# Kernel optimization log

Hardware: AMD Instinct MI355X
Metric: run time of the kernel (lower is better)

## Reference

```python
import jax, jax.numpy as jnp
import numpy as np

N = 50000       # nodes
E = 800000      # directed edges (src -> dst)
INDIM, HID, OUT = 256, 128, 64
NEG_SLOPE = 0.2  # PyG GATConv default negative_slope


def gat_layer(x, src, dst, W, a_src, a_dst, b, n_nodes):
    """Single-head PyG-style GATConv with self-loops already in (src, dst)."""
    h = x @ W.T                                   # [N, F_out]
    alpha_src = h @ a_src                         # [N]
    alpha_dst = h @ a_dst                         # [N]
    # per-edge attention logits, LeakyReLU
    e = jax.nn.leaky_relu(alpha_src[src] + alpha_dst[dst], NEG_SLOPE)  # [E']
    # segment softmax grouped by destination node (numerically stable)
    m = jnp.full((n_nodes,), -jnp.inf, e.dtype).at[dst].max(e)
    ee = jnp.exp(e - m[dst])
    denom = jax.ops.segment_sum(ee, dst, num_segments=n_nodes)
    alpha = ee / denom[dst]                       # [E']
    # weighted scatter-add of source messages
    out = jax.ops.segment_sum(h[src] * alpha[:, None], dst, num_segments=n_nodes)
    return out + b


def setup_inputs() -> dict:
    key = jax.random.key(0)
    ks = jax.random.split(key, 10)
    s = 0.1
    return {
        "x": jax.random.normal(ks[0], (N, INDIM), jnp.float32),
        "edge_index": jax.random.randint(ks[1], (2, E), 0, N, dtype=jnp.int32),
        "W1": jax.random.normal(ks[2], (HID, INDIM), jnp.float32) * s,
        "a_src1": jax.random.normal(ks[3], (HID,), jnp.float32) * s,
        "a_dst1": jax.random.normal(ks[4], (HID,), jnp.float32) * s,
        "b1": jnp.zeros((HID,), jnp.float32),
        "W2": jax.random.normal(ks[5], (OUT, HID), jnp.float32) * s,
        "a_src2": jax.random.normal(ks[6], (OUT,), jnp.float32) * s,
        "a_dst2": jax.random.normal(ks[7], (OUT,), jnp.float32) * s,
        "b2": jnp.zeros((OUT,), jnp.float32),
    }


def reference(x, edge_index, W1, a_src1, a_dst1, b1, W2, a_src2, a_dst2, b2):
    n_nodes = x.shape[0]
    # PyG GATConv default add_self_loops=True
    loops = jnp.arange(n_nodes, dtype=edge_index.dtype)
    src = jnp.concatenate([edge_index[0], loops])
    dst = jnp.concatenate([edge_index[1], loops])
    h = gat_layer(x, src, dst, W1, a_src1, a_dst1, b1, n_nodes)
    h = jax.nn.relu(h)
    h = gat_layer(h, src, dst, W2, a_src2, a_dst2, b2, n_nodes)
    return h
```

## Files before the change

kernel.cpp:

```cpp
#include <hip/hip_runtime.h>
#include <hip/hip_bf16.h>
#include <math.h>

#define NN 50000
#define EE 800000
#define INDIM 256
#define HID 128
#define OUTF 64
#define NEG_SLOPE 0.2f
#define CAP 64

#define NB ((NN + 255) >> 8)
#define BCAP 6144
#define CHUNK 2048
#define EPT 8
#define BPAD 16

typedef __attribute__((ext_vector_type(8))) short bf16x8;
typedef __attribute__((ext_vector_type(4))) float f32x4;

__device__ inline float bflo(unsigned p) { return __uint_as_float(p << 16); }
__device__ inline float bfhi(unsigned p) { return __uint_as_float(p & 0xffff0000u); }
__device__ inline unsigned f2bf(float f) {
    unsigned u = __float_as_uint(f);
    return (u + 0x7fffu + ((u >> 16) & 1u)) >> 16;
}
__device__ inline unsigned cvt_pk_bf16(float lo, float hi) {
    unsigned r;
    asm("v_cvt_pk_bf16_f32 %0, %1, %2" : "=v"(r) : "v"(lo), "v"(hi));
    return r;
}
__device__ inline float leaky(float l) { return (l > 0.f) ? l : NEG_SLOPE * l; }

template <typename AT, int BM, int BN, int WR, int WC, bool FAL>
__device__ inline void gemm_body(const AT* __restrict__ A,
                                 const float* __restrict__ B,
                                 unsigned short* __restrict__ Cb,
                                 const float* __restrict__ a_s,
                                 const float* __restrict__ a_d,
                                 float* __restrict__ asrc,
                                 float* __restrict__ adst,
                                 int N, int K, int bid)
{
    constexpr int LD = 40;
    constexpr int MF = (BM / WR) / 16;
    constexpr int NF = (BN / WC) / 16;
    constexpr int NA  = (sizeof(AT) == 4) ? (BM * 8 / 256) : (BM * 4 / 256);
    constexpr int NBL = BN * 8 / 256;
    __shared__ unsigned short As[BM * LD];
    __shared__ unsigned short Bs[BN * LD];
    __shared__ float al_s[FAL ? 2 * BM : 2];

    const int tid = threadIdx.x;
    const int wave = tid >> 6, lane = tid & 63;
    const int wr = wave / WC, wc = wave % WC;
    const int wrow0 = wr * (BM / WR);
    const int wcol0 = wc * (BN / WC);
    const int row0 = bid * BM;
    const int lrow = lane & 15, lkg = lane >> 4;

    if constexpr (FAL) {
        for (int i = tid; i < 2 * BM; i += 256) al_s[i] = 0.f;
    }

    int arow[NA], aoff[NA]; bool aval[NA];
    #pragma unroll
    for (int u = 0; u < NA; ++u) {
        int i = u * 256 + tid;
        if constexpr (sizeof(AT) == 4) { arow[u] = i >> 3; aoff[u] = (i & 7) * 4; }
        else                           { arow[u] = i >> 2; aoff[u] = (i & 3) * 8; }
        aval[u] = (row0 + arow[u]) < N;
    }
    int brow[NBL], boff[NBL];
    #pragma unroll
    for (int u = 0; u < NBL; ++u) {
        int i = u * 256 + tid;
        brow[u] = i >> 3; boff[u] = (i & 7) * 4;
    }

    uint4 ra[NA], rb[NBL];
    auto loadA = [&](int k0) {
        #pragma unroll
        for (int u = 0; u < NA; ++u) {
            ra[u] = make_uint4(0u, 0u, 0u, 0u);
            if (aval[u])
                ra[u] = *(const uint4*)((const AT*)A + (size_t)(row0 + arow[u]) * K + k0 + aoff[u]);
        }
    };
    auto loadB = [&](int k0) {
        #pragma unroll
        for (int u = 0; u < NBL; ++u)
            rb[u] = *(const uint4*)(B + (size_t)brow[u] * K + k0 + boff[u]);
    };
    auto storeLDS = [&]() {
        if constexpr (sizeof(AT) == 4) {
            #pragma unroll
            for (int u = 0; u < NA; ++u) {
                unsigned p0 = cvt_pk_bf16(__uint_as_float(ra[u].x), __uint_as_float(ra[u].y));
                unsigned p1 = cvt_pk_bf16(__uint_as_float(ra[u].z), __uint_as_float(ra[u].w));
                *(uint2*)&As[arow[u] * LD + aoff[u]] = make_uint2(p0, p1);
            }
        } else {
            #pragma unroll
            for (int u = 0; u < NA; ++u)
                *(uint4*)&As[arow[u] * LD + aoff[u]] = ra[u];
        }
        #pragma unroll
        for (int u = 0; u < NBL; ++u) {
            unsigned p0 = cvt_pk_bf16(__uint_as_float(rb[u].x), __uint_as_float(rb[u].y));
            unsigned p1 = cvt_pk_bf16(__uint_as_float(rb[u].z), __uint_as_float(rb[u].w));
            *(uint2*)&Bs[brow[u] * LD + boff[u]] = make_uint2(p0, p1);
        }
    };

    f32x4 acc[MF][NF];
    #pragma unroll
    for (int mi = 0; mi < MF; ++mi)
        #pragma unroll
        for (int ni = 0; ni < NF; ++ni) acc[mi][ni] = 0.f;

    const int NK = K / 32;
    loadA(0); loadB(0);
    for (int ks = 0; ks < NK; ++ks) {
        storeLDS();
        __syncthreads();
        if (ks + 1 < NK) { loadA((ks + 1) * 32); loadB((ks + 1) * 32); }

        bf16x8 af[MF], bfr[NF];
        #pragma unroll
        for (int mi = 0; mi < MF; ++mi)
            af[mi] = *(const bf16x8*)&As[(wrow0 + mi * 16 + lrow) * LD + lkg * 8];
        #pragma unroll
        for (int ni = 0; ni < NF; ++ni)
            bfr[ni] = *(const bf16x8*)&Bs[(wcol0 + ni * 16 + lrow) * LD + lkg * 8];
        #pragma unroll
        for (int mi = 0; mi < MF; ++mi)
            #pragma unroll
            for (int ni = 0; ni < NF; ++ni)
                acc[mi][ni] = __builtin_amdgcn_mfma_f32_16x16x32_bf16(
                    af[mi], bfr[ni], acc[mi][ni], 0, 0, 0);
        __syncthreads();
    }

    if constexpr (FAL) {
        float asv[NF], adv[NF];
        #pragma unroll
        for (int ni = 0; ni < NF; ++ni) {
            int c = wcol0 + ni * 16 + lrow;
            asv[ni] = a_s[c]; adv[ni] = a_d[c];
        }
        #pragma unroll
        for (int mi = 0; mi < MF; ++mi)
            #pragma unroll
            for (int r = 0; r < 4; ++r) {
                float ps = 0.f, pd = 0.f;
                #pragma unroll
                for (int ni = 0; ni < NF; ++ni) {
                    ps = fmaf(acc[mi][ni][r], asv[ni], ps);
                    pd = fmaf(acc[mi][ni][r], adv[ni], pd);
                }
                #pragma unroll
                for (int d = 1; d < 16; d <<= 1) {
                    ps += __shfl_xor(ps, d);
                    pd += __shfl_xor(pd, d);
                }
                int lr_ = wrow0 + mi * 16 + lkg * 4 + r;
                if (lrow == 0) {
                    atomicAdd(&al_s[lr_], ps);
                    atomicAdd(&al_s[BM + lr_], pd);
                }
            }
    }

    #pragma unroll
    for (int mi = 0; mi < MF; ++mi)
        #pragma unroll
        for (int ni = 0; ni < NF; ++ni)
            #pragma unroll
            for (int r = 0; r < 4; ++r) {
                int gr = row0 + wrow0 + mi * 16 + lkg * 4 + r;
                int gc = wcol0 + ni * 16 + lrow;
                if (gr < N)
                    Cb[(size_t)gr * BN + gc] = (unsigned short)f2bf(acc[mi][ni][r]);
            }

    if constexpr (FAL) {
        __syncthreads();
        if (tid < BM) {
            int gr = row0 + tid;
            if (gr < N) { asrc[gr] = al_s[tid]; adst[gr] = al_s[BM + tid]; }
        }
    }
}

__device__ inline void bin_body(int bb,
                                const int* __restrict__ src_in,
                                const int* __restrict__ dst_in,
                                unsigned* __restrict__ gbucket,
                                int* __restrict__ bcnt,
                                int E, int tot)
{
    __shared__ int h_hist[256];
    __shared__ int h_scan[256];
    __shared__ int h_ofs[256];
    __shared__ int h_gbase[256];
    __shared__ unsigned grp[CHUNK];

    const int tid = threadIdx.x;
    const int e0 = bb * CHUNK;
    const int cntc = min(CHUNK, tot - e0);

    h_hist[tid] = 0;
    __syncthreads();

    unsigned pk[EPT];
    bool val[EPT];
    #pragma unroll
    for (int u = 0; u < EPT; ++u) {
        int e = e0 + u * 256 + tid;
        val[u] = (e < tot);
        if (val[u]) {
            int d, s;
            if (e < E) { d = dst_in[e]; s = src_in[e]; }
            else       { d = e - E;    s = d; }
            pk[u] = ((unsigned)d << 16) | (unsigned)s;
            atomicAdd(&h_hist[d >> 8], 1);
        }
    }
    __syncthreads();

    int v = h_hist[tid];
    int incl = v;
    h_scan[tid] = incl;
    __syncthreads();
    for (int off = 1; off < 256; off <<= 1) {
        int t = (tid >= off) ? h_scan[tid - off] : 0;
        __syncthreads();
        incl += t;
        h_scan[tid] = incl;
        __syncthreads();
    }
    int excl = incl - v;
    h_scan[tid] = excl;
    h_ofs[tid] = excl;
    h_gbase[tid] = (tid < NB && v > 0) ? atomicAdd(&bcnt[tid * BPAD], v) : 0;
    __syncthreads();

    #pragma unroll
    for (int u = 0; u < EPT; ++u)
        if (val[u]) {
            int b = pk[u] >> 24;
            int pos = atomicAdd(&h_ofs[b], 1);
            grp[pos] = pk[u];
        }
    __syncthreads();

    for (int i = tid; i < cntc; i += 256) {
        unsigned p = grp[i];
        int b = p >> 24;
        int gp = h_gbase[b] + (i - h_scan[b]);
        if (gp < BCAP) gbucket[(size_t)b * BCAP + gp] = p;
    }
}

__global__ __launch_bounds__(256) void fused_gemm1_bin(
    const float* __restrict__ x, const float* __restrict__ W1,
    unsigned short* __restrict__ h1b,
    const float* __restrict__ a_s, const float* __restrict__ a_d,
    float* __restrict__ asrc, float* __restrict__ adst,
    const int* __restrict__ src_in, const int* __restrict__ dst_in,
    unsigned* __restrict__ gbucket, int* __restrict__ bcnt,
    int N, int K, int GB, int E)
{
    if ((int)blockIdx.x < GB) {
        gemm_body<float, 64, 128, 2, 2, true>(x, W1, h1b, a_s, a_d,
                                              asrc, adst, N, K, blockIdx.x);
    } else {
        bin_body(blockIdx.x - GB, src_in, dst_in, gbucket, bcnt, E, E + N);
    }
}

__global__ __launch_bounds__(256) void csr_build(
    const unsigned* __restrict__ gbucket, const int* __restrict__ bcnt,
    int* __restrict__ cnt, unsigned short* __restrict__ csr, int N)
{
    __shared__ int c2[256];
    __shared__ unsigned short cl[256 * CAP];

    const int b = blockIdx.x;
    const int tid = threadIdx.x;
    c2[tid] = 0;
    __syncthreads();

    int len = bcnt[b * BPAD];
    if (len > BCAP) len = BCAP;
    for (int i = tid; i < len; i += 256) {
        unsigned p = gbucket[(size_t)b * BCAP + i];
        int dl = (p >> 16) & 255;
        int s  = p & 0xffff;
        int r = atomicAdd(&c2[dl], 1);
        if (r < CAP) cl[(dl << 6) + r] = (unsigned short)s;
    }
    __syncthreads();

    int d = (b << 8) + tid;
    if (d < N) cnt[d] = c2[tid];

    int rows = N - (b << 8);
    rows = (rows > 256) ? 256 : rows;
    const uint4* sp = (const uint4*)cl;
    uint4* dp = (uint4*)(csr + (((size_t)b << 8) << 6));
    for (int i = tid; i < rows * 8; i += 256) dp[i] = sp[i];
}

__global__ __launch_bounds__(256) void agg1_gemm2_kernel(
    const unsigned short* __restrict__ h1b, const unsigned short* __restrict__ csr,
    const int* __restrict__ cnt_arr, const float* __restrict__ asrc1,
    const float* __restrict__ adst1, const float* __restrict__ b1,
    const float* __restrict__ W2, const float* __restrict__ a_s2,
    const float* __restrict__ a_d2, unsigned short* __restrict__ h2b,
    float* __restrict__ asrc2, float* __restrict__ adst2, int N)
{
    constexpr int F = HID, G = 16, EPI = 4, STEP = 16;
    constexpr int LDH = 136;
    __shared__ unsigned short hm[64 * LDH];
    __shared__ unsigned short Bs[64 * 40];

    const int tid = threadIdx.x;
    const int wv = tid >> 6, lane = tid & 63;
    const int base = (int)blockIdx.x * 64;
    const int grp = lane / G, fl = lane % G;

    float bs[8];
    *(float4*)&bs[0] = *(const float4*)(b1 + fl * 8);
    *(float4*)&bs[4] = *(const float4*)(b1 + fl * 8 + 4);

    for (int i = 0; i < 16; ++i) {
        const int row = i * 4 + wv;
        const int node = base + row;
        float acc[8];
        #pragma unroll
        for (int p = 0; p < 8; ++p) acc[p] = 0.f;

        if (node < N) {
            const size_t beg = (size_t)node << 6;
            int cntv = cnt_arr[node];
            cntv = (cntv > CAP) ? CAP : cntv;
            const float ad = adst1[node];

            int s = 0;
            float e = 0.f;
            if (lane < cntv) { s = (int)csr[beg + lane]; e = __expf(leaky(asrc1[s] + ad)); }
            float denom = e;
            #pragma unroll
            for (int d = 32; d > 0; d >>= 1) denom += __shfl_xor(denom, d);
            float w = e * __fdividef(1.f, denom);

            for (int jj0 = 0; jj0 < cntv; jj0 += STEP) {
                uint4 q[4];
                float wj[4];
                #pragma unroll
                for (int u = 0; u < 4; ++u) {
                    int sel = jj0 + u * EPI + grp;
                    int sj = __shfl(s, sel);
                    wj[u] = __shfl(w, sel);
                    q[u] = make_uint4(0u, 0u, 0u, 0u);
                    if (sel < cntv)
                        q[u] = *(const uint4*)(h1b + (size_t)sj * F + fl * 8);
                }
                #pragma unroll
                for (int u = 0; u < 4; ++u) {
                    acc[0] += wj[u] * bflo(q[u].x); acc[1] += wj[u] * bfhi(q[u].x);
                    acc[2] += wj[u] * bflo(q[u].y); acc[3] += wj[u] * bfhi(q[u].y);
                    acc[4] += wj[u] * bflo(q[u].z); acc[5] += wj[u] * bfhi(q[u].z);
                    acc[6] += wj[u] * bflo(q[u].w); acc[7] += wj[u] * bfhi(q[u].w);
                }
            }
            #pragma unroll
            for (int d = G; d < 64; d <<= 1)
                #pragma unroll
                for (int p = 0; p < 8; ++p) acc[p] += __shfl_xor(acc[p], d);

            #pragma unroll
            for (int p = 0; p < 8; ++p) acc[p] = fmaxf(acc[p] + bs[p], 0.f);
        }
        if (lane < G) {
            uint4 pk;
            pk.x = cvt_pk_bf16(acc[0], acc[1]);
            pk.y = cvt_pk_bf16(acc[2], acc[3]);
            pk.z = cvt_pk_bf16(acc[4], acc[5]);
            pk.w = cvt_pk_bf16(acc[6], acc[7]);
            *(uint4*)&hm[row * LDH + lane * 8] = pk;
        }
    }
    __syncthreads();

    const int lrow = lane & 15, lkg = lane >> 4;
    f32x4 acc2[4];
    #pragma unroll
    for (int ni = 0; ni < 4; ++ni) acc2[ni] = 0.f;

    for (int k0 = 0; k0 < HID; k0 += 32) {
        #pragma unroll
        for (int it = tid; it < 64 * 8; it += 256) {
            int rw = it >> 3, kq = it & 7;
            float4 v = *(const float4*)(W2 + (size_t)rw * HID + k0 + kq * 4);
            unsigned p0 = cvt_pk_bf16(v.x, v.y);
            unsigned p1 = cvt_pk_bf16(v.z, v.w);
            *(uint2*)&Bs[rw * 40 + kq * 4] = make_uint2(p0, p1);
        }
        __syncthreads();
        bf16x8 af = *(const bf16x8*)&hm[(wv * 16 + lrow) * LDH + k0 + lkg * 8];
        #pragma unroll
        for (int ni = 0; ni < 4; ++ni) {
            bf16x8 bfr = *(const bf16x8*)&Bs[(ni * 16 + lrow) * 40 + lkg * 8];
            acc2[ni] = __builtin_amdgcn_mfma_f32_16x16x32_bf16(af, bfr, acc2[ni], 0, 0, 0);
        }
        __syncthreads();
    }

    float asv[4], adv[4];
    #pragma unroll
    for (int ni = 0; ni < 4; ++ni) {
        int c = ni * 16 + lrow;
        asv[ni] = a_s2[c]; adv[ni] = a_d2[c];
    }
    #pragma unroll
    for (int r = 0; r < 4; ++r) {
        float ps = 0.f, pd = 0.f;
        #pragma unroll
        for (int ni = 0; ni < 4; ++ni) {
            ps = fmaf(acc2[ni][r], asv[ni], ps);
            pd = fmaf(acc2[ni][r], adv[ni], pd);
        }
        #pragma unroll
        for (int d = 1; d < 16; d <<= 1) {
            ps += __shfl_xor(ps, d);
            pd += __shfl_xor(pd, d);
        }
        int gr = base + wv * 16 + lkg * 4 + r;
        if (lrow == 0 && gr < N) { asrc2[gr] = ps; adst2[gr] = pd; }
    }

    #pragma unroll
    for (int ni = 0; ni < 4; ++ni)
        #pragma unroll
        for (int r = 0; r < 4; ++r) {
            int gr = base + wv * 16 + lkg * 4 + r;
            int gc = ni * 16 + lrow;
            if (gr < N)
                h2b[(size_t)gr * OUTF + gc] = (unsigned short)f2bf(acc2[ni][r]);
        }
}

template <int F, bool RELU, bool OUTBF>
__global__ __launch_bounds__(256) void aggregate_kernel(
    const unsigned short* __restrict__ hb, const unsigned short* __restrict__ csr,
    const int* __restrict__ cnt_arr, const float* __restrict__ asrc,
    const float* __restrict__ adst, const float* __restrict__ bias,
    void* __restrict__ outv, int n)
{
    constexpr int G = F / 8;
    constexpr int EPI = 64 / G;
    constexpr int STEP = EPI * 4;
    int wave = (int)((blockIdx.x * (size_t)blockDim.x + threadIdx.x) >> 6);
    int lane = threadIdx.x & 63;
    if (wave >= n) return;
    const size_t beg = (size_t)wave << 6;
    int cntv = cnt_arr[wave];
    cntv = (cntv > CAP) ? CAP : cntv;
    const float ad = adst[wave];
    const int grp = lane / G, fl = lane % G;

    float acc[8];
    #pragma unroll
    for (int p = 0; p < 8; ++p) acc[p] = 0.f;

    int s = 0;
    float e = 0.f;
    if (lane < cntv) { s = (int)csr[beg + lane]; e = __expf(leaky(asrc[s] + ad)); }
    float denom = e;
    #pragma unroll
    for (int d = 32; d > 0; d >>= 1) denom += __shfl_xor(denom, d);
    float w = e * __fdividef(1.f, denom);

    for (int jj0 = 0; jj0 < cntv; jj0 += STEP) {
        uint4 q[4];
        float wj[4];
        #pragma unroll
        for (int u = 0; u < 4; ++u) {
            int sel = jj0 + u * EPI + grp;
            int sj = __shfl(s, sel);
            wj[u] = __shfl(w, sel);
            q[u] = make_uint4(0u, 0u, 0u, 0u);
            if (sel < cntv)
                q[u] = *(const uint4*)(hb + (size_t)sj * F + fl * 8);
        }
        #pragma unroll
        for (int u = 0; u < 4; ++u) {
            acc[0] += wj[u] * bflo(q[u].x); acc[1] += wj[u] * bfhi(q[u].x);
            acc[2] += wj[u] * bflo(q[u].y); acc[3] += wj[u] * bfhi(q[u].y);
            acc[4] += wj[u] * bflo(q[u].z); acc[5] += wj[u] * bfhi(q[u].z);
            acc[6] += wj[u] * bflo(q[u].w); acc[7] += wj[u] * bfhi(q[u].w);
        }
    }

    #pragma unroll
    for (int d = G; d < 64; d <<= 1)
        #pragma unroll
        for (int p = 0; p < 8; ++p) acc[p] += __shfl_xor(acc[p], d);

    if (lane < G) {
        float v[8];
        #pragma unroll
        for (int p = 0; p < 8; ++p) {
            v[p] = acc[p] + bias[fl * 8 + p];
            if (RELU) v[p] = fmaxf(v[p], 0.f);
        }
        if constexpr (OUTBF) {
            unsigned short* o = (unsigned short*)outv + (size_t)wave * F + fl * 8;
            uint4 pk;
            pk.x = cvt_pk_bf16(v[0], v[1]);
            pk.y = cvt_pk_bf16(v[2], v[3]);
            pk.z = cvt_pk_bf16(v[4], v[5]);
            pk.w = cvt_pk_bf16(v[6], v[7]);
            *(uint4*)o = pk;
        } else {
            float* o = (float*)outv + (size_t)wave * F + fl * 8;
            *(float4*)o       = make_float4(v[0], v[1], v[2], v[3]);
            *(float4*)(o + 4) = make_float4(v[4], v[5], v[6], v[7]);
        }
    }
}

extern "C" void kernel_launch(void* const* d_in, const int* in_sizes, int n_in,
                              void* d_out, int out_size, void* d_ws, size_t ws_size,
                              hipStream_t stream)
{
    const float* x      = (const float*)d_in[0];
    const int*   ei     = (const int*)d_in[1];
    const float* W1     = (const float*)d_in[2];
    const float* a_src1 = (const float*)d_in[3];
    const float* a_dst1 = (const float*)d_in[4];
    const float* b1     = (const float*)d_in[5];
    const float* W2     = (const float*)d_in[6];
    const float* a_src2 = (const float*)d_in[7];
    const float* a_dst2 = (const float*)d_in[8];
    const float* b2     = (const float*)d_in[9];
    float* out = (float*)d_out;

    const int N = NN, E = EE;
    const int* src_in = ei;
    const int* dst_in = ei + E;

    char* p = (char*)d_ws;
    unsigned short* h1b   = (unsigned short*)p; p += (size_t)N * HID * 2;
    unsigned short* h2b   = (unsigned short*)p; p += (size_t)N * OUTF * 2;
    float* asrc  = (float*)p; p += (size_t)N * 4;
    float* adst  = (float*)p; p += (size_t)N * 4;
    float* asrc2 = (float*)p; p += (size_t)N * 4;
    float* adst2 = (float*)p; p += (size_t)N * 4;
    int* cnt    = (int*)p;   p += (size_t)N * 4;
    unsigned short* csr = (unsigned short*)p; p += (size_t)N * CAP * 2;
    int* bcnt = (int*)p; p += (size_t)NB * BPAD * 4;
    unsigned* gbucket = (unsigned*)h2b;

    hipMemsetAsync(bcnt, 0, (size_t)NB * BPAD * 4, stream);

    const int GB   = (N + 63) / 64;
    const int BINB = (E + N + CHUNK - 1) / CHUNK;
    const int nwb  = (N * 64 + 255) / 256;

    fused_gemm1_bin<<<GB + BINB, 256, 0, stream>>>(
        x, W1, h1b, a_src1, a_dst1, asrc, adst, src_in, dst_in,
        gbucket, bcnt, N, INDIM, GB, E);
    csr_build<<<NB, 256, 0, stream>>>(gbucket, bcnt, cnt, csr, N);

    agg1_gemm2_kernel<<<GB, 256, 0, stream>>>(
        h1b, csr, cnt, asrc, adst, b1, W2, a_src2, a_dst2,
        h2b, asrc2, adst2, N);

    aggregate_kernel<OUTF, false, false><<<nwb, 256, 0, stream>>>(
        h2b, csr, cnt, asrc2, adst2, b2, out, N);

    (void)in_sizes; (void)n_in; (void)out_size; (void)ws_size;
}
```

Baseline: 203.7 us.

## Precompute layer-1 softmax weights in CSR build and halve agg1 block rows

The CSR build kernel now computes the per-edge exponentiated attention logits and per-destination denominators for layer 1 in shared memory. It writes normalized weights to a new float buffer laid out like the CSR. The layer-1 aggregation kernel then loads these weights instead of gathering asrc and recomputing the softmax with wave reductions. Separately, the fused agg1+GEMM2 kernel processes 32 nodes per block instead of 64, splitting the MFMA output columns across waves and combining the attention dot products through shared-memory atomics. This trades an extra 12.8 MB weight buffer write and read, plus higher LDS use in csr_build, for less per-node work and more blocks in the aggregation kernel.

```diff
diff --git a/kernel.cpp b/kernel.cpp
--- a/kernel.cpp
+++ b/kernel.cpp
@@ -282,14 +282,22 @@
 
 __global__ __launch_bounds__(256) void csr_build(
     const unsigned* __restrict__ gbucket, const int* __restrict__ bcnt,
-    int* __restrict__ cnt, unsigned short* __restrict__ csr, int N)
+    const float* __restrict__ asrc1, const float* __restrict__ adst1,
+    int* __restrict__ cnt, unsigned short* __restrict__ csr,
+    float* __restrict__ wcsr, int N)
 {
     __shared__ int c2[256];
+    __shared__ float den[256];
+    __shared__ float ads[256];
     __shared__ unsigned short cl[256 * CAP];
+    __shared__ float el[256 * CAP];
 
     const int b = blockIdx.x;
     const int tid = threadIdx.x;
+    const int dg = (b << 8) + tid;
     c2[tid] = 0;
+    den[tid] = 0.f;
+    ads[tid] = (dg < N) ? adst1[dg] : 0.f;
     __syncthreads();
 
     int len = bcnt[b * BPAD];
@@ -298,44 +306,59 @@
         unsigned p = gbucket[(size_t)b * BCAP + i];
         int dl = (p >> 16) & 255;
         int s  = p & 0xffff;
+        float e = __expf(leaky(asrc1[s] + ads[dl]));
         int r = atomicAdd(&c2[dl], 1);
-        if (r < CAP) cl[(dl << 6) + r] = (unsigned short)s;
-    }
-    __syncthreads();
-
-    int d = (b << 8) + tid;
-    if (d < N) cnt[d] = c2[tid];
+        if (r < CAP) {
+            cl[(dl << 6) + r] = (unsigned short)s;
+            el[(dl << 6) + r] = e;
+        }
+        atomicAdd(&den[dl], e);
+    }
+    __syncthreads();
+
+    if (dg < N) cnt[dg] = c2[tid];
 
     int rows = N - (b << 8);
     rows = (rows > 256) ? 256 : rows;
+
+    for (int i = tid; i < rows * CAP; i += 256)
+        el[i] = __fdividef(el[i], den[i >> 6]);
+    __syncthreads();
+
     const uint4* sp = (const uint4*)cl;
     uint4* dp = (uint4*)(csr + (((size_t)b << 8) << 6));
     for (int i = tid; i < rows * 8; i += 256) dp[i] = sp[i];
+    const uint4* wp = (const uint4*)el;
+    uint4* dq = (uint4*)(wcsr + (((size_t)b << 8) << 6));
+    for (int i = tid; i < rows * 16; i += 256) dq[i] = wp[i];
 }
 
 __global__ __launch_bounds__(256) void agg1_gemm2_kernel(
     const unsigned short* __restrict__ h1b, const unsigned short* __restrict__ csr,
-    const int* __restrict__ cnt_arr, const float* __restrict__ asrc1,
-    const float* __restrict__ adst1, const float* __restrict__ b1,
+    const int* __restrict__ cnt_arr, const float* __restrict__ wcsr,
+    const float* __restrict__ b1,
     const float* __restrict__ W2, const float* __restrict__ a_s2,
     const float* __restrict__ a_d2, unsigned short* __restrict__ h2b,
     float* __restrict__ asrc2, float* __restrict__ adst2, int N)
 {
     constexpr int F = HID, G = 16, EPI = 4, STEP = 16;
     constexpr int LDH = 136;
-    __shared__ unsigned short hm[64 * LDH];
+    __shared__ unsigned short hm[32 * LDH];
     __shared__ unsigned short Bs[64 * 40];
+    __shared__ float al2[64];
 
     const int tid = threadIdx.x;
     const int wv = tid >> 6, lane = tid & 63;
-    const int base = (int)blockIdx.x * 64;
+    const int base = (int)blockIdx.x * 32;
     const int grp = lane / G, fl = lane % G;
+
+    if (tid < 64) al2[tid] = 0.f;
 
     float bs[8];
     *(float4*)&bs[0] = *(const float4*)(b1 + fl * 8);
     *(float4*)&bs[4] = *(const float4*)(b1 + fl * 8 + 4);
 
-    for (int i = 0; i < 16; ++i) {
+    for (int i = 0; i < 8; ++i) {
         const int row = i * 4 + wv;
         const int node = base + row;
         float acc[8];
@@ -346,15 +369,10 @@
             const size_t beg = (size_t)node << 6;
             int cntv = cnt_arr[node];
             cntv = (cntv > CAP) ? CAP : cntv;
-            const float ad = adst1[node];
 
             int s = 0;
-            float e = 0.f;
-            if (lane < cntv) { s = (int)csr[beg + lane]; e = __expf(leaky(asrc1[s] + ad)); }
-            float denom = e;
-            #pragma unroll
-            for (int d = 32; d > 0; d >>= 1) denom += __shfl_xor(denom, d);
-            float w = e * __fdividef(1.f, denom);
+            float w = 0.f;
+            if (lane < cntv) { s = (int)csr[beg + lane]; w = wcsr[beg + lane]; }
 
             for (int jj0 = 0; jj0 < cntv; jj0 += STEP) {
                 uint4 q[4];
@@ -395,10 +413,11 @@
     }
     __syncthreads();
 
+    const int wr = wv >> 1, wc = wv & 1;
     const int lrow = lane & 15, lkg = lane >> 4;
-    f32x4 acc2[4];
-    #pragma unroll
-    for (int ni = 0; ni < 4; ++ni) acc2[ni] = 0.f;
+    f32x4 acc2[2];
+    #pragma unroll
+    for (int ni = 0; ni < 2; ++ni) acc2[ni] = 0.f;
 
     for (int k0 = 0; k0 < HID; k0 += 32) {
         #pragma unroll
@@ -410,26 +429,26 @@
             *(uint2*)&Bs[rw * 40 + kq * 4] = make_uint2(p0, p1);
         }
         __syncthreads();
-        bf16x8 af = *(const bf16x8*)&hm[(wv * 16 + lrow) * LDH + k0 + lkg * 8];
-        #pragma unroll
-        for (int ni = 0; ni < 4; ++ni) {
-            bf16x8 bfr = *(const bf16x8*)&Bs[(ni * 16 + lrow) * 40 + lkg * 8];
+        bf16x8 af = *(const bf16x8*)&hm[(wr * 16 + lrow) * LDH + k0 + lkg * 8];
+        #pragma unroll
+        for (int ni = 0; ni < 2; ++ni) {
+            bf16x8 bfr = *(const bf16x8*)&Bs[(wc * 32 + ni * 16 + lrow) * 40 + lkg * 8];
             acc2[ni] = __builtin_amdgcn_mfma_f32_16x16x32_bf16(af, bfr, acc2[ni], 0, 0, 0);
         }
         __syncthreads();
     }
 
-    float asv[4], adv[4];
-    #pragma unroll
-    for (int ni = 0; ni < 4; ++ni) {
-        int c = ni * 16 + lrow;
+    float asv[2], adv[2];
+    #pragma unroll
+    for (int ni = 0; ni < 2; ++ni) {
+        int c = wc * 32 + ni * 16 + lrow;
         asv[ni] = a_s2[c]; adv[ni] = a_d2[c];
     }
     #pragma unroll
     for (int r = 0; r < 4; ++r) {
         float ps = 0.f, pd = 0.f;
         #pragma unroll
-        for (int ni = 0; ni < 4; ++ni) {
+        for (int ni = 0; ni < 2; ++ni) {
             ps = fmaf(acc2[ni][r], asv[ni], ps);
             pd = fmaf(acc2[ni][r], adv[ni], pd);
         }
@@ -438,16 +457,24 @@
             ps += __shfl_xor(ps, d);
             pd += __shfl_xor(pd, d);
         }
-        int gr = base + wv * 16 + lkg * 4 + r;
-        if (lrow == 0 && gr < N) { asrc2[gr] = ps; adst2[gr] = pd; }
-    }
-
-    #pragma unroll
-    for (int ni = 0; ni < 4; ++ni)
+        int lr_ = wr * 16 + lkg * 4 + r;
+        if (lrow == 0) {
+            atomicAdd(&al2[lr_], ps);
+            atomicAdd(&al2[32 + lr_], pd);
+        }
+    }
+    __syncthreads();
+    if (tid < 32) {
+        int gr = base + tid;
+        if (gr < N) { asrc2[gr] = al2[tid]; adst2[gr] = al2[32 + tid]; }
+    }
+
+    #pragma unroll
+    for (int ni = 0; ni < 2; ++ni)
         #pragma unroll
         for (int r = 0; r < 4; ++r) {
-            int gr = base + wv * 16 + lkg * 4 + r;
-            int gc = ni * 16 + lrow;
+            int gr = base + wr * 16 + lkg * 4 + r;
+            int gc = wc * 32 + ni * 16 + lrow;
             if (gr < N)
                 h2b[(size_t)gr * OUTF + gc] = (unsigned short)f2bf(acc2[ni][r]);
         }
@@ -562,6 +589,7 @@
     float* adst2 = (float*)p; p += (size_t)N * 4;
     int* cnt    = (int*)p;   p += (size_t)N * 4;
     unsigned short* csr = (unsigned short*)p; p += (size_t)N * CAP * 2;
+    float* wcsr = (float*)p; p += (size_t)N * CAP * 4;
     int* bcnt = (int*)p; p += (size_t)NB * BPAD * 4;
     unsigned* gbucket = (unsigned*)h2b;
 
@@ -569,15 +597,17 @@
 
     const int GB   = (N + 63) / 64;
     const int BINB = (E + N + CHUNK - 1) / CHUNK;
+    const int GBA  = (N + 31) / 32;
     const int nwb  = (N * 64 + 255) / 256;
 
     fused_gemm1_bin<<<GB + BINB, 256, 0, stream>>>(
         x, W1, h1b, a_src1, a_dst1, asrc, adst, src_in, dst_in,
         gbucket, bcnt, N, INDIM, GB, E);
-    csr_build<<<NB, 256, 0, stream>>>(gbucket, bcnt, cnt, csr, N);
-
-    agg1_gemm2_kernel<<<GB, 256, 0, stream>>>(
-        h1b, csr, cnt, asrc, adst, b1, W2, a_src2, a_dst2,
+    csr_build<<<NB, 256, 0, stream>>>(gbucket, bcnt, asrc, adst,
+                                      cnt, csr, wcsr, N);
+
+    agg1_gemm2_kernel<<<GBA, 256, 0, stream>>>(
+        h1b, csr, cnt, wcsr, b1, W2, a_src2, a_dst2,
         h2b, asrc2, adst2, N);
 
     aggregate_kernel<OUTF, false, false><<<nwb, 256, 0, stream>>>(
```

Result: slower. 209.3 us (+2.8%).
